# Kernel tuning notes

Measured on AMD Instinct MI355X. Metric: run time of the kernel, lower is better.

## Reference

```python
import jax, jax.numpy as jnp
import numpy as np

T = 4096        # sequence length
D = 128         # input feature dim
TRACE = 64      # trace_size
CONTEXT = 64    # context_size
HID = 64        # internal dense width (hardcoded 64 in module)
OUT = 128       # output_size
LN_EPS = 1e-6   # flax LayerNorm default epsilon


def setup_inputs() -> dict:
    key = jax.random.key(0)
    ks = jax.random.split(key, 12)

    def dense(k, fi, fo):
        return (jax.random.normal(k, (fi, fo), jnp.float32) / np.sqrt(fi).astype(np.float32))

    inp = {}
    inp["x"] = jax.random.normal(ks[0], (T, D), jnp.float32)
    inp["state"] = jnp.zeros((1, TRACE, CONTEXT), jnp.complex64)
    inp["start"] = jax.random.uniform(ks[1], (T,)) < 0.01  # sparse episode resets
    # deterministic FFM decay / frequency params (init_deterministic)
    inp["a"] = jnp.linspace(1e-6, 0.5, TRACE).astype(jnp.float32)
    inp["b"] = (2.0 * jnp.pi / jnp.linspace(1.0, 1000.0, CONTEXT)).astype(jnp.float32)
    inp["W1"] = dense(ks[2], D, HID);               inp["b1"] = jnp.zeros((HID,), jnp.float32)
    inp["W2"] = dense(ks[3], HID, 2 * TRACE);       inp["b2"] = jnp.zeros((2 * TRACE,), jnp.float32)
    inp["Wgi"] = dense(ks[4], 2 * TRACE, TRACE);    inp["bgi"] = jnp.zeros((TRACE,), jnp.float32)
    inp["Wp"] = dense(ks[5], 2 * TRACE, TRACE);     inp["bp"] = jnp.zeros((TRACE,), jnp.float32)
    inp["Wz"] = dense(ks[6], 2 * TRACE * CONTEXT, HID); inp["bz"] = jnp.zeros((HID,), jnp.float32)
    inp["Wgo"] = dense(ks[7], 2 * TRACE, HID);      inp["bgo"] = jnp.zeros((HID,), jnp.float32)
    inp["Ws"] = dense(ks[8], 2 * TRACE, HID);       inp["bs"] = jnp.zeros((HID,), jnp.float32)
    inp["W3"] = dense(ks[9], HID, HID);             inp["b3"] = jnp.zeros((HID,), jnp.float32)
    inp["W4"] = dense(ks[10], HID, OUT);            inp["b4"] = jnp.zeros((OUT,), jnp.float32)
    return inp


def _ffm_scan(scan_in, state0, start, a, b):
    # scan_in: (T, TRACE, CONTEXT) float, state0: (1, TRACE, CONTEXT) complex64
    t = scan_in.shape[0]
    timestep = jnp.ones((t + 1, 1, 1), dtype=jnp.int32)
    start_f = jnp.concatenate(
        [jnp.zeros((1, 1, 1), dtype=bool), start.reshape(t, 1, 1)], axis=0)
    xs = jnp.concatenate([state0, scan_in.astype(jnp.complex64)], axis=0)

    neg_a = -jnp.abs(a).reshape(1, TRACE, 1)
    b_r = b.reshape(1, 1, CONTEXT)
    ab = neg_a + 1j * b_r  # (1, TRACE, CONTEXT) complex

    def gamma(j):
        # j: (N,1,1) int -> (N, TRACE, CONTEXT) complex decay
        return jnp.exp(ab * j.astype(jnp.float32))

    def combine(carry, incoming):
        prev_start, s, i = carry
        st, xx, j = incoming
        keep = jnp.logical_not(st)
        s = s * keep
        j = j * keep.astype(j.dtype)
        new_s = s * gamma(j) + xx
        return (jnp.logical_or(st, prev_start), new_s, j + i)

    _, new_state, _ = jax.lax.associative_scan(
        combine, (start_f, xs, timestep), axis=0)
    return new_state[1:]  # (T, TRACE, CONTEXT) complex64


def _layernorm(x):
    mu = jnp.mean(x, axis=-1, keepdims=True)
    var = jnp.var(x, axis=-1, keepdims=True)
    return (x - mu) * jax.lax.rsqrt(var + LN_EPS)


def _forward(x, state, start, a, b, W1, b1, W2, b2, Wgi, bgi, Wp, bp,
             Wz, bz, Wgo, bgo, Ws, bs, W3, b3, W4, b4):
    h = jax.nn.relu(x @ W1 + b1)                 # (T, 64)
    h2 = h @ W2 + b2                             # (T, 2*TRACE)
    gate_in = jax.nn.sigmoid(h2 @ Wgi + bgi)     # (T, TRACE)
    pre = jax.nn.sigmoid(h2 @ Wp + bp)           # (T, TRACE)
    gated = pre * gate_in                        # (T, TRACE)
    scan_in = jnp.broadcast_to(gated[:, :, None], (gated.shape[0], TRACE, CONTEXT))
    state_seq = _ffm_scan(scan_in, state, start, a, b)  # (T, TRACE, CONTEXT) c64
    z_in = jnp.concatenate([jnp.real(state_seq), jnp.imag(state_seq)],
                           axis=-1).reshape(state_seq.shape[0], -1)
    z = z_in @ Wz + bz                           # (T, 64)
    gate_out = jax.nn.sigmoid(h2 @ Wgo + bgo)    # (T, 64)
    skip = h2 @ Ws + bs                          # (T, 64)
    out = _layernorm(z * gate_out) + skip * (1.0 - gate_out)
    out = jax.nn.relu(out @ W3 + b3)
    out = out @ W4 + b4                          # (T, OUT)
    return out, state_seq[-1:]


def reference(x, state, start, a, b, W1, b1, W2, b2, Wgi, bgi, Wp, bp,
              Wz, bz, Wgo, bgo, Ws, bs, W3, b3, W4, b4):
    return _forward(x, state, start, a, b, W1, b1, W2, b2, Wgi, bgi, Wp, bp,
                    Wz, bz, Wgo, bgo, Ws, bs, W3, b3, W4, b4)
```

## Files before the change

### kernel.cpp

```cpp
#include <hip/hip_runtime.h>
#include <math.h>

#define T_LEN 4096
#define D_IN 128
#define KDIM 4096
#define K2   8192

#define OFF_GATED 0u
#define OFF_GO    262144u
#define OFF_SKIP  524288u
#define OFF_PART  786432u
#define OFF_FLAGS 4980736u
#define OFF_CHS   4984832u
#define OFF_WZT   4984896u
#define OFF_SCR   5247040u

typedef __attribute__((ext_vector_type(8))) short short8v;
typedef __attribute__((ext_vector_type(4))) float float4v;

__device__ __forceinline__ float sigm(float x){ return 1.f/(1.f+expf(-x)); }
__device__ __forceinline__ unsigned short f2bf(float x){
    unsigned int u = __float_as_uint(x);
    return (unsigned short)((u + 0x7FFFu + ((u >> 16) & 1u)) >> 16);
}
__device__ __forceinline__ float wsum(float v) {
#pragma unroll
    for (int o = 32; o; o >>= 1) v += __shfl_xor(v, o, 64);
    return v;
}

__global__ __launch_bounds__(512) void k_prep(
    const unsigned char* __restrict__ su8, const int* __restrict__ si32,
    int* __restrict__ flags, int* __restrict__ chunkStart,
    const float* __restrict__ Wz, unsigned short* __restrict__ wzt,
    const float* __restrict__ x,
    const float* __restrict__ W1, const float* __restrict__ b1,
    const float* __restrict__ W2, const float* __restrict__ b2,
    const float* __restrict__ Wgi, const float* __restrict__ bgi,
    const float* __restrict__ Wp,  const float* __restrict__ bp,
    const float* __restrict__ Wgo, const float* __restrict__ bgo,
    const float* __restrict__ Wsk, const float* __restrict__ bsk,
    float* __restrict__ gated, float* __restrict__ go, float* __restrict__ sk)
{
    const int bx = blockIdx.x;
    const int tid = threadIdx.x;

    if (bx == 0) {
        __shared__ int cnt;
        if (tid == 0) cnt = 0;
        __syncthreads();
        int local = 0;
        for (int i = tid; i < 4096; i += 512)
            if (i & 3) local += su8[i];
        if (local) atomicAdd(&cnt, local);
        __syncthreads();
        if (cnt > 0) { for (int i = tid; i < 4096; i += 512) flags[i] = su8[i] ? 1 : 0; }
        else         { for (int i = tid; i < 4096; i += 512) flags[i] = si32[i] ? 1 : 0; }
        __syncthreads();
        if (tid < 64) {
            int any = 0;
#pragma unroll 8
            for (int j = 0; j < 64; ++j) any |= flags[tid * 64 + j];
            chunkStart[tid] = any;
        }
        return;
    }
    if (bx <= 64) {
        int idx = ((bx - 1) * 512 + tid) * 16;
        int j = idx >> 13, k0 = idx & 8191;
#pragma unroll
        for (int e = 0; e < 16; ++e) {
            int k = k0 + e;
            wzt[(size_t)j * K2 + k] = f2bf(Wz[(size_t)k * 64 + j]);
        }
        return;
    }

    __shared__ float xs[8][128];
    __shared__ float hs[8][64];
    __shared__ float h2s[8][128];
    __shared__ float tmp[8][4][64];
    const int t0 = (bx - 65) * 8;

    if (tid < 256) {
        int r = tid >> 5, kq = (tid & 31) << 2;
        *(float4*)&xs[r][kq] = *(const float4*)&x[(size_t)(t0 + r) * D_IN + kq];
    }

    const int j1 = tid >> 3, ks1 = tid & 7;
    float wr1[16];
#pragma unroll
    for (int kk = 0; kk < 16; ++kk) wr1[kk] = W1[(size_t)(ks1 * 16 + kk) * 64 + j1];
    const float bias1 = b1[j1];
    __syncthreads();
#pragma unroll
    for (int r = 0; r < 8; ++r) {
        float p = 0.f;
#pragma unroll
        for (int kq = 0; kq < 4; ++kq) {
            float4 xv = *(const float4*)&xs[r][ks1 * 16 + kq * 4];
            p += xv.x*wr1[kq*4] + xv.y*wr1[kq*4+1] + xv.z*wr1[kq*4+2] + xv.w*wr1[kq*4+3];
        }
        p += __shfl_xor(p, 1, 64); p += __shfl_xor(p, 2, 64); p += __shfl_xor(p, 4, 64);
        if (ks1 == 0) hs[r][j1] = fmaxf(p + bias1, 0.f);
    }
    __syncthreads();

    const int j2 = tid >> 2, ks2 = tid & 3;
    float wr2[16];
#pragma unroll
    for (int kk = 0; kk < 16; ++kk) wr2[kk] = W2[(size_t)(ks2 * 16 + kk) * 128 + j2];
    const float bias2 = b2[j2];
#pragma unroll
    for (int r = 0; r < 8; ++r) {
        float p = 0.f;
#pragma unroll
        for (int kq = 0; kq < 4; ++kq) {
            float4 hv = *(const float4*)&hs[r][ks2 * 16 + kq * 4];
            p += hv.x*wr2[kq*4] + hv.y*wr2[kq*4+1] + hv.z*wr2[kq*4+2] + hv.w*wr2[kq*4+3];
        }
        p += __shfl_xor(p, 1, 64); p += __shfl_xor(p, 2, 64);
        if (ks2 == 0) h2s[r][j2] = p + bias2;
    }
    __syncthreads();

    const int mat = tid >> 7, jj = (tid & 127) >> 1, kh = tid & 1;
    const float* Wm = (mat == 0) ? Wgi : (mat == 1) ? Wp : (mat == 2) ? Wgo : Wsk;
    float wgr[64];
#pragma unroll
    for (int kk = 0; kk < 64; ++kk) wgr[kk] = Wm[(size_t)(kh * 64 + kk) * 64 + jj];
#pragma unroll
    for (int r = 0; r < 8; ++r) {
        float p = 0.f;
#pragma unroll
        for (int kq = 0; kq < 16; ++kq) {
            float4 hv = *(const float4*)&h2s[r][kh * 64 + kq * 4];
            p += hv.x*wgr[kq*4] + hv.y*wgr[kq*4+1] + hv.z*wgr[kq*4+2] + hv.w*wgr[kq*4+3];
        }
        p += __shfl_xor(p, 1, 64);
        if (kh == 0) tmp[r][mat][jj] = p;
    }
    __syncthreads();

    {
        int r = tid >> 6, j = tid & 63;
        int t = t0 + r;
        float gi = sigm(tmp[r][0][j] + bgi[j]);
        float pr = sigm(tmp[r][1][j] + bp[j]);
        float g  = sigm(tmp[r][2][j] + bgo[j]);
        float s  = tmp[r][3][j] + bsk[j];
        gated[t * 64 + j] = gi * pr;
        go[t * 64 + j]    = g;
        sk[t * 64 + j]    = s;
    }
}

__global__ __launch_bounds__(512) void k_scanA(
    const float* __restrict__ gated, const int* __restrict__ flags,
    const float* __restrict__ a, const float* __restrict__ b,
    float2* __restrict__ carryB)
{
    const int p = threadIdx.x >> 6, c = threadIdx.x & 63;
    const int pair = blockIdx.x * 8 + p;
    const int ch = pair & 63, m = pair >> 6;
    const int t0 = ch * 64;

    const double ead = exp(-fabs((double)a[m]));
    const double bbd = (double)b[c];
    const float lre = (float)(ead * cos(bbd)), lim = (float)(ead * sin(bbd));
    float gv = gated[(size_t)(t0 + c) * 64 + m];
    unsigned long long fmask = __ballot(flags[t0 + c] != 0);
    float sre = 0.f, sim = 0.f;
#pragma unroll 8
    for (int j = 0; j < 64; ++j) {
        float g = __shfl(gv, j, 64);
        if ((fmask >> j) & 1) { sre = g; sim = 0.f; }
        else {
            float nr = fmaf(sre, lre, fmaf(-sim, lim, g));
            float ni = fmaf(sre, lim, sim * lre);
            sre = nr; sim = ni;
        }
    }
    carryB[(size_t)ch * KDIM + m * 64 + c] = make_float2(sre, sim);
}

__global__ __launch_bounds__(256) void k_scanBZ2(
    const float* __restrict__ gated, const int* __restrict__ flags,
    const int* __restrict__ chs,
    const float* __restrict__ a, const float* __restrict__ b,
    const float* __restrict__ st0,
    const float2* __restrict__ carryB,
    const unsigned short* __restrict__ wzt,
    float* __restrict__ part,
    float* __restrict__ out)
{
    const int tid = threadIdx.x;
    const int ml = tid >> 6, c = tid & 63;
    const int chpair = blockIdx.x & 31, mg = blockIdx.x >> 5;
    const int ch0 = chpair * 2;
    const int m = mg * 4 + ml;
    __shared__ unsigned short st[64 * 512];

    const double ead = exp(-fabs((double)a[m]));
    const double bbd = (double)b[c];
    const float lre = (float)(ead * cos(bbd)), lim = (float)(ead * sin(bbd));

    unsigned long long cmask = __ballot(chs[c] != 0);
    const double ea64 = exp(-64.0 * fabs((double)a[m]));
    const float l64re = (float)(ea64 * cos(64.0 * bbd));
    const float l64im = (float)(ea64 * sin(64.0 * bbd));
    float cre = st0[(m * 64 + c) * 2];
    float cim = st0[(m * 64 + c) * 2 + 1];
    {
        const float2* cbase = carryB + m * 64 + c;
        float2 BA[16], BB[16];
#define LOADB(dst, base)                                          \
        _Pragma("unroll")                                         \
        for (int q = 0; q < 16; ++q)                              \
            dst[q] = cbase[(size_t)((base) + q) * KDIM];
#define COMB(src, base)                                           \
        _Pragma("unroll")                                         \
        for (int q = 0; q < 16; ++q) {                            \
            int chp = (base) + q;                                 \
            if (chp < ch0) {      \
                if ((cmask >> chp) & 1) { cre = src[q].x; cim = src[q].y; } \
                else {                                            \
                    float nr = fmaf(cre, l64re, fmaf(-cim, l64im, src[q].x)); \
                    float ni = fmaf(cre, l64im, fmaf(cim, l64re, src[q].y)); \
                    cre = nr; cim = ni;                           \
                }                                                 \
            }                                                     \
        }
        if (ch0 > 0)  { LOADB(BA, 0) }
        if (ch0 > 16) { LOADB(BB, 16) }
        if (ch0 > 0)  { COMB(BA, 0) }
        if (ch0 > 32) { LOADB(BA, 32) }
        if (ch0 > 16) { COMB(BB, 16) }
        if (ch0 > 48) { LOADB(BB, 48) }
        if (ch0 > 32) { COMB(BA, 32) }
        if (ch0 > 48) { COMB(BB, 48) }
#undef LOADB
#undef COMB
    }

    const int l = c;
    const int jrow = ml * 16 + (l & 15);
    short8v bfr[16];
#pragma unroll
    for (int ks = 0; ks < 16; ++ks)
        bfr[ks] = *(const short8v*)&wzt[(size_t)jrow * K2 + mg * 512 + (ks * 4 + (l >> 4)) * 8];

    const int e0 = ml * 128 + c, e1 = e0 + 64;
    const int jcol = ml * 16 + (l & 15);

    for (int u = 0; u < 2; ++u) {
        const int ch = ch0 + u, t0s = ch * 64;

        float gv = gated[(size_t)(t0s + c) * 64 + m];
        unsigned long long fmask = __ballot(flags[t0s + c] != 0);
#pragma unroll 4
        for (int j = 0; j < 64; ++j) {
            float g = __shfl(gv, j, 64);
            if ((fmask >> j) & 1) { cre = g; cim = 0.f; }
            else {
                float nr = fmaf(cre, lre, fmaf(-cim, lim, g));
                float ni = fmaf(cre, lim, cim * lre);
                cre = nr; cim = ni;
            }
            const int sx = (j & 7) << 3;
            st[j * 512 + (e0 ^ sx)] = f2bf(cre);
            st[j * 512 + (e1 ^ sx)] = f2bf(cim);
        }
        if (ch == 63) {
            out[524288 + m * 64 + c]        = cre;
            out[524288 + 4096 + m * 64 + c] = cim;
        }
        __syncthreads();

        float4v acc[4];
#pragma unroll
        for (int i = 0; i < 4; ++i) acc[i] = (float4v){0.f, 0.f, 0.f, 0.f};
#pragma unroll
        for (int ks = 0; ks < 16; ++ks) {
#pragma unroll
            for (int mt = 0; mt < 4; ++mt) {
                const int row = mt * 16 + (l & 15);
                const int rchunk = (ks * 4 + (l >> 4)) ^ (row & 7);
                short8v af = *(const short8v*)&st[row * 512 + rchunk * 8];
                acc[mt] = __builtin_amdgcn_mfma_f32_16x16x32_bf16(af, bfr[ks], acc[mt], 0, 0, 0);
            }
        }

        float* pp = part + (size_t)mg * 262144;
#pragma unroll
        for (int mt = 0; mt < 4; ++mt) {
            const int trow = t0s + mt * 16 + (l >> 4) * 4;
#pragma unroll
            for (int r = 0; r < 4; ++r)
                pp[(size_t)(trow + r) * 64 + jcol] = acc[mt][r];
        }
        __syncthreads();
    }
}

__global__ __launch_bounds__(256) void k_epi(
    const float* __restrict__ part, const float* __restrict__ bz,
    const float* __restrict__ go, const float* __restrict__ sk,
    const float* __restrict__ W3, const float* __restrict__ b3,
    const float* __restrict__ W4, const float* __restrict__ b4,
    float* __restrict__ out)
{
    __shared__ float ob[4][64], hb[4][64];
    const int w = threadIdx.x >> 6, j = threadIdx.x & 63;
    const int t = blockIdx.x * 4 + w;
    float z = bz[j];
#pragma unroll
    for (int p = 0; p < 16; ++p) z += part[(size_t)p * 262144 + t * 64 + j];
    float g = go[t * 64 + j];
    float y = z * g;
    float mu = wsum(y) * 0.015625f;
    float d = y - mu;
    float var = wsum(d * d) * 0.015625f;
    float o = d * (1.f / sqrtf(var + 1e-6f)) + sk[t * 64 + j] * (1.f - g);
    ob[w][j] = o;
    __syncthreads();
    float acc = b3[j];
#pragma unroll 8
    for (int k = 0; k < 64; ++k) acc += ob[w][k] * W3[k * 64 + j];
    hb[w][j] = fmaxf(acc, 0.f);
    __syncthreads();
    float o1 = b4[j], o2 = b4[j + 64];
#pragma unroll 8
    for (int k = 0; k < 64; ++k) { float hv = hb[w][k]; o1 += hv * W4[k * 128 + j]; o2 += hv * W4[k * 128 + j + 64]; }
    out[(size_t)t * 128 + j] = o1;
    out[(size_t)t * 128 + j + 64] = o2;
}

extern "C" void kernel_launch(void* const* d_in, const int* in_sizes, int n_in,
                              void* d_out, int out_size, void* d_ws, size_t ws_size,
                              hipStream_t stream)
{
    const float* x   = (const float*)d_in[0];
    const float* st0 = (const float*)d_in[1];
    const void*  start = d_in[2];
    const float* a  = (const float*)d_in[3];
    const float* b  = (const float*)d_in[4];
    const float* W1 = (const float*)d_in[5];  const float* b1 = (const float*)d_in[6];
    const float* W2 = (const float*)d_in[7];  const float* b2 = (const float*)d_in[8];
    const float* Wgi= (const float*)d_in[9];  const float* bgi= (const float*)d_in[10];
    const float* Wp = (const float*)d_in[11]; const float* bp = (const float*)d_in[12];
    const float* Wz = (const float*)d_in[13]; const float* bz = (const float*)d_in[14];
    const float* Wgo= (const float*)d_in[15]; const float* bgo= (const float*)d_in[16];
    const float* Wsk= (const float*)d_in[17]; const float* bsk= (const float*)d_in[18];
    const float* W3 = (const float*)d_in[19]; const float* b3 = (const float*)d_in[20];
    const float* W4 = (const float*)d_in[21]; const float* b4 = (const float*)d_in[22];

    float* ws    = (float*)d_ws;
    float* out   = (float*)d_out;
    float* gated = ws + OFF_GATED;
    float* go    = ws + OFF_GO;
    float* sk    = ws + OFF_SKIP;
    float* part  = ws + OFF_PART;
    int*   flags = (int*)(ws + OFF_FLAGS);
    int*   chs   = (int*)(ws + OFF_CHS);
    unsigned short* wzt = (unsigned short*)(ws + OFF_WZT);
    float2* carryB = (float2*)(ws + OFF_SCR);

    hipLaunchKernelGGL(k_prep, dim3(577), dim3(512), 0, stream,
                       (const unsigned char*)start, (const int*)start, flags, chs,
                       Wz, wzt, x, W1, b1, W2, b2, Wgi, bgi, Wp, bp,
                       Wgo, bgo, Wsk, bsk, gated, go, sk);
    hipLaunchKernelGGL(k_scanA, dim3(512), dim3(512), 0, stream,
                       gated, flags, a, b, carryB);
    hipLaunchKernelGGL(k_scanBZ2, dim3(512), dim3(256), 0, stream,
                       gated, flags, chs, a, b, st0, carryB, wzt, part, out);
    hipLaunchKernelGGL(k_epi, dim3(1024), dim3(256), 0, stream,
                       part, bz, go, sk, W3, b3, W4, b4, out);
}
```

Measured before the change: 76.71 us.

## Keep MLP weights in registers in epilogue and hoist carry loads earlier

The epilogue kernel now handles 16 timesteps per block instead of 4. Each thread keeps a slice of W3/W4 in registers and computes dot products over a split K, reduced with cross-lane shuffles. This reuses the weights across rows rather than rereading them from global memory for every row. In the scan kernel, the first carry-buffer loads are issued before the double-precision exp/sin/cos setup so their latency overlaps that math. Costs are higher register pressure and fewer blocks in the epilogue.

```diff
diff --git a/kernel.cpp b/kernel.cpp
--- a/kernel.cpp
+++ b/kernel.cpp
@@ -201,47 +201,47 @@
     const int m = mg * 4 + ml;
     __shared__ unsigned short st[64 * 512];
 
+    const float2* cbase = carryB + m * 64 + c;
+    float2 BA[16], BB[16];
+#define LOADB(dst, base)                                          \
+    _Pragma("unroll")                                             \
+    for (int q = 0; q < 16; ++q)                                  \
+        dst[q] = cbase[(size_t)((base) + q) * KDIM];
+    if (ch0 > 0)  { LOADB(BA, 0) }
+    if (ch0 > 16) { LOADB(BB, 16) }
+
+    float cre = st0[(m * 64 + c) * 2];
+    float cim = st0[(m * 64 + c) * 2 + 1];
+    unsigned long long cmask = __ballot(chs[c] != 0);
+
     const double ead = exp(-fabs((double)a[m]));
     const double bbd = (double)b[c];
     const float lre = (float)(ead * cos(bbd)), lim = (float)(ead * sin(bbd));
-
-    unsigned long long cmask = __ballot(chs[c] != 0);
     const double ea64 = exp(-64.0 * fabs((double)a[m]));
     const float l64re = (float)(ea64 * cos(64.0 * bbd));
     const float l64im = (float)(ea64 * sin(64.0 * bbd));
-    float cre = st0[(m * 64 + c) * 2];
-    float cim = st0[(m * 64 + c) * 2 + 1];
-    {
-        const float2* cbase = carryB + m * 64 + c;
-        float2 BA[16], BB[16];
-#define LOADB(dst, base)                                          \
-        _Pragma("unroll")                                         \
-        for (int q = 0; q < 16; ++q)                              \
-            dst[q] = cbase[(size_t)((base) + q) * KDIM];
+
 #define COMB(src, base)                                           \
-        _Pragma("unroll")                                         \
-        for (int q = 0; q < 16; ++q) {                            \
-            int chp = (base) + q;                                 \
-            if (chp < ch0) {      \
-                if ((cmask >> chp) & 1) { cre = src[q].x; cim = src[q].y; } \
-                else {                                            \
-                    float nr = fmaf(cre, l64re, fmaf(-cim, l64im, src[q].x)); \
-                    float ni = fmaf(cre, l64im, fmaf(cim, l64re, src[q].y)); \
-                    cre = nr; cim = ni;                           \
-                }                                                 \
+    _Pragma("unroll")                                             \
+    for (int q = 0; q < 16; ++q) {                                \
+        int chp = (base) + q;                                     \
+        if (chp < ch0) {          \
+            if ((cmask >> chp) & 1) { cre = src[q].x; cim = src[q].y; } \
+            else {                                                \
+                float nr = fmaf(cre, l64re, fmaf(-cim, l64im, src[q].x)); \
+                float ni = fmaf(cre, l64im, fmaf(cim, l64re, src[q].y)); \
+                cre = nr; cim = ni;                               \
             }                                                     \
-        }
-        if (ch0 > 0)  { LOADB(BA, 0) }
-        if (ch0 > 16) { LOADB(BB, 16) }
-        if (ch0 > 0)  { COMB(BA, 0) }
-        if (ch0 > 32) { LOADB(BA, 32) }
-        if (ch0 > 16) { COMB(BB, 16) }
-        if (ch0 > 48) { LOADB(BB, 48) }
-        if (ch0 > 32) { COMB(BA, 32) }
-        if (ch0 > 48) { COMB(BB, 48) }
+        }                                                         \
+    }
+    if (ch0 > 0)  { COMB(BA, 0) }
+    if (ch0 > 32) { LOADB(BA, 32) }
+    if (ch0 > 16) { COMB(BB, 16) }
+    if (ch0 > 48) { LOADB(BB, 48) }
+    if (ch0 > 32) { COMB(BA, 32) }
+    if (ch0 > 48) { COMB(BB, 48) }
 #undef LOADB
 #undef COMB
-    }
 
     const int l = c;
     const int jrow = ml * 16 + (l & 15);
@@ -310,30 +310,62 @@
     const float* __restrict__ W4, const float* __restrict__ b4,
     float* __restrict__ out)
 {
-    __shared__ float ob[4][64], hb[4][64];
-    const int w = threadIdx.x >> 6, j = threadIdx.x & 63;
-    const int t = blockIdx.x * 4 + w;
-    float z = bz[j];
-#pragma unroll
-    for (int p = 0; p < 16; ++p) z += part[(size_t)p * 262144 + t * 64 + j];
-    float g = go[t * 64 + j];
-    float y = z * g;
-    float mu = wsum(y) * 0.015625f;
-    float d = y - mu;
-    float var = wsum(d * d) * 0.015625f;
-    float o = d * (1.f / sqrtf(var + 1e-6f)) + sk[t * 64 + j] * (1.f - g);
-    ob[w][j] = o;
-    __syncthreads();
-    float acc = b3[j];
-#pragma unroll 8
-    for (int k = 0; k < 64; ++k) acc += ob[w][k] * W3[k * 64 + j];
-    hb[w][j] = fmaxf(acc, 0.f);
-    __syncthreads();
-    float o1 = b4[j], o2 = b4[j + 64];
-#pragma unroll 8
-    for (int k = 0; k < 64; ++k) { float hv = hb[w][k]; o1 += hv * W4[k * 128 + j]; o2 += hv * W4[k * 128 + j + 64]; }
-    out[(size_t)t * 128 + j] = o1;
-    out[(size_t)t * 128 + j + 64] = o2;
+    __shared__ float ob[16][64], hb[16][64];
+    const int tid = threadIdx.x;
+    const int w = tid >> 6, j = tid & 63;
+    const int tbase = blockIdx.x * 16;
+
+    const int j3 = tid >> 2, ks3 = tid & 3;
+    float wgr3[16];
+#pragma unroll
+    for (int kk = 0; kk < 16; ++kk) wgr3[kk] = W3[(size_t)(ks3 * 16 + kk) * 64 + j3];
+    const float b3v = b3[j3];
+    const int j4 = tid >> 1, kh = tid & 1;
+    float wgr4[32];
+#pragma unroll
+    for (int kk = 0; kk < 32; ++kk) wgr4[kk] = W4[(size_t)(kh * 32 + kk) * 128 + j4];
+    const float b4v = b4[j4];
+
+#pragma unroll
+    for (int it = 0; it < 4; ++it) {
+        const int r = it * 4 + w;
+        const int t = tbase + r;
+        float z = bz[j];
+#pragma unroll
+        for (int p = 0; p < 16; ++p) z += part[(size_t)p * 262144 + t * 64 + j];
+        float g = go[t * 64 + j];
+        float y = z * g;
+        float mu = wsum(y) * 0.015625f;
+        float d = y - mu;
+        float var = wsum(d * d) * 0.015625f;
+        ob[r][j] = d * (1.f / sqrtf(var + 1e-6f)) + sk[t * 64 + j] * (1.f - g);
+    }
+    __syncthreads();
+
+#pragma unroll
+    for (int r = 0; r < 16; ++r) {
+        float p = 0.f;
+#pragma unroll
+        for (int kq = 0; kq < 4; ++kq) {
+            float4 v = *(const float4*)&ob[r][ks3 * 16 + kq * 4];
+            p += v.x*wgr3[kq*4] + v.y*wgr3[kq*4+1] + v.z*wgr3[kq*4+2] + v.w*wgr3[kq*4+3];
+        }
+        p += __shfl_xor(p, 1, 64); p += __shfl_xor(p, 2, 64);
+        if (ks3 == 0) hb[r][j3] = fmaxf(p + b3v, 0.f);
+    }
+    __syncthreads();
+
+#pragma unroll
+    for (int r = 0; r < 16; ++r) {
+        float p = 0.f;
+#pragma unroll
+        for (int kq = 0; kq < 8; ++kq) {
+            float4 v = *(const float4*)&hb[r][kh * 32 + kq * 4];
+            p += v.x*wgr4[kq*4] + v.y*wgr4[kq*4+1] + v.z*wgr4[kq*4+2] + v.w*wgr4[kq*4+3];
+        }
+        p += __shfl_xor(p, 1, 64);
+        if (kh == 0) out[(size_t)(tbase + r) * 128 + j4] = p + b4v;
+    }
 }
 
 extern "C" void kernel_launch(void* const* d_in, const int* in_sizes, int n_in,
@@ -374,6 +406,6 @@
                        gated, flags, a, b, carryB);
     hipLaunchKernelGGL(k_scanBZ2, dim3(512), dim3(256), 0, stream,
                        gated, flags, chs, a, b, st0, carryB, wzt, part, out);
-    hipLaunchKernelGGL(k_epi, dim3(1024), dim3(256), 0, stream,
+    hipLaunchKernelGGL(k_epi, dim3(256), dim3(256), 0, stream,
                        part, bz, go, sk, W3, b3, W4, b4, out);
 }
```

New measurement: 78.07 us. Within noise of the previous version (+1.8%).
